# Kernel optimization log

Measured on AMD Instinct MI355X. Metric: run time of the kernel, lower is better.

The kernel has to match this reference:

```python
import jax, jax.numpy as jnp
import numpy as np

BLOCK_K = 32   # BLOCK_K_SIZE_MIN in the original Triton kernel
BLOCK_N = 32   # output-block granularity of the hash


def _hash_indices(random_numbers, num_nb, num_kb, num_red_kb):
    # universal hash of (n_block, k_block) -> reduced k-block index
    r = random_numbers.astype(jnp.uint32)
    nb = jnp.arange(num_nb, dtype=jnp.uint32)[:, None]
    kb = jnp.arange(num_kb, dtype=jnp.uint32)[None, :]
    hv = (kb * r[0] + nb * r[1] + r[2]) ^ r[3]
    return (hv % jnp.uint32(num_red_kb)).astype(jnp.int32)  # [num_nb, num_kb]


def _ssl_forward(x, weight, bias, random_numbers):
    orig_shape = x.shape
    K = orig_shape[-1]
    x2 = x.reshape(-1, K)                       # [M, K]
    N, red_K = weight.shape
    num_kb = K // BLOCK_K
    num_red_kb = red_K // BLOCK_K
    num_nb = N // BLOCK_N
    h = _hash_indices(random_numbers, num_nb, num_kb, num_red_kb)  # [num_nb, num_kb]
    # Gather the virtual full weight from the reduced weight via hash indices.
    wb = weight.reshape(num_nb, BLOCK_N, num_red_kb, BLOCK_K)
    w_full = jnp.take_along_axis(wb, h[:, None, :, None], axis=2)  # [num_nb, BN, num_kb, BK]
    w_full = w_full.reshape(N, K)
    y = x2 @ w_full.T
    if bias is not None:
        y = y + bias
    return y.reshape(*orig_shape[:-1], N)


def setup_inputs() -> dict:
    key = jax.random.key(0)
    k1, k2, k3 = jax.random.split(key, 3)
    in_features, out_features, redn_factor, seed = 8192, 512, 8, 1024
    red_in = ((in_features // redn_factor + BLOCK_K - 1) // BLOCK_K) * BLOCK_K  # 1024
    x = jax.random.normal(k1, (4, 2048, in_features), dtype=jnp.float32)
    bound = 1.0 / np.sqrt(red_in)
    weight = jax.random.uniform(k2, (out_features, red_in), jnp.float32, -bound, bound)
    bias = jax.random.uniform(k3, (out_features,), jnp.float32, -bound, bound)
    rng = np.random.default_rng(seed)
    random_numbers = jnp.asarray(rng.integers(1, 2**31 - 1, size=4), dtype=jnp.int32)
    return {"x": x, "weight": weight, "bias": bias,
            "random_numbers": random_numbers, "redn_factor": redn_factor}


def reference(x, weight, bias, random_numbers, redn_factor):
    return _ssl_forward(x, weight, bias, random_numbers)
```

## Files before the change

kernel.cpp:

```cpp
#include <hip/hip_runtime.h>
#include <hip/hip_bf16.h>
#include <stdint.h>


typedef __bf16 bf16x4_t __attribute__((ext_vector_type(4)));
typedef __bf16 bf16x8_t __attribute__((ext_vector_type(8)));
typedef float f32x4 __attribute__((ext_vector_type(4)));

#define BM 128
#define BN 128
#define BK 32
#define LDSK 40
#define KSPLIT 4

__global__ void init_out(float* __restrict__ Out, const float* __restrict__ Bias,
                         int N, int total4) {
  int i = blockIdx.x * blockDim.x + threadIdx.x;
  if (i < total4) {
    int idx = i << 2;
    int n = idx % N;
    *(f32x4*)(Out + idx) = *(const f32x4*)(Bias + n);
  }
}

__global__ __launch_bounds__(256, 1) void ssl_gemm(
    const float* __restrict__ X,
    const float* __restrict__ W,
    const int* __restrict__ RN,
    float* __restrict__ Out,
    int M, int N, int K, int redK, uint32_t numRedKb, int mTiles, int nTiles) {
  __shared__ __align__(16) __bf16 As[BM * LDSK];
  __shared__ __align__(16) __bf16 Bs[BN * LDSK];

  const uint32_t r0 = (uint32_t)RN[0], r1 = (uint32_t)RN[1];
  const uint32_t r2 = (uint32_t)RN[2], r3 = (uint32_t)RN[3];
  const uint32_t redMask = numRedKb - 1u;
  const bool pow2 = (numRedKb & (numRedKb - 1u)) == 0u;

  const int id = blockIdx.x;
  const int mTile = id % mTiles;
  const int rest = id / mTiles;
  const int nTile = rest % nTiles;
  const int kChunk = rest / nTiles;

  const int tid = threadIdx.x;
  const int wave = tid >> 6;
  const int lane = tid & 63;
  const int wm = wave >> 1, wn = wave & 1;

  const int lRow = tid >> 3;
  const int lCol = (tid & 7) << 2;
  const float* aBase = X + (size_t)(mTile * BM + lRow) * K + lCol;
  const float* bBase = W + (size_t)(nTile * BN + lRow) * redK + lCol;

  auto loadA = [&](int kb, f32x4* r) {
    const float* p = aBase + (size_t)kb * BK;
#pragma unroll
    for (int i = 0; i < 4; ++i)
      r[i] = *(const f32x4*)(p + (size_t)(i * 32) * K);
  };
  auto loadB = [&](int kb, f32x4* r) {
    const uint32_t kk = (uint32_t)kb * r0 + r2;
#pragma unroll
    for (int i = 0; i < 4; ++i) {
      const uint32_t nb = (uint32_t)(nTile * (BN / 32) + i);
      const uint32_t hv = (kk + nb * r1) ^ r3;
      const uint32_t h = pow2 ? (hv & redMask) : (hv % numRedKb);
      r[i] = *(const f32x4*)(bBase + (size_t)(i * 32) * redK + h * 32u);
    }
  };
  auto stage = [&](const f32x4* rA, const f32x4* rB) {
#pragma unroll
    for (int i = 0; i < 4; ++i) {
      bf16x4_t a, b;
#pragma unroll
      for (int j = 0; j < 4; ++j) {
        a[j] = (__bf16)rA[i][j];
        b[j] = (__bf16)rB[i][j];
      }
      *(bf16x4_t*)&As[(i * 32 + lRow) * LDSK + lCol] = a;
      *(bf16x4_t*)&Bs[(i * 32 + lRow) * LDSK + lCol] = b;
    }
  };

  f32x4 acc[4][4] = {};
  auto compute = [&]() {
    bf16x8_t af[4], bfr[4];
    const int kOff = (lane >> 4) << 3;
    const int r16 = lane & 15;
#pragma unroll
    for (int mi = 0; mi < 4; ++mi)
      af[mi] = *(const bf16x8_t*)&As[((wm << 6) + (mi << 4) + r16) * LDSK + kOff];
#pragma unroll
    for (int ni = 0; ni < 4; ++ni)
      bfr[ni] = *(const bf16x8_t*)&Bs[((wn << 6) + (ni << 4) + r16) * LDSK + kOff];
#pragma unroll
    for (int mi = 0; mi < 4; ++mi)
#pragma unroll
      for (int ni = 0; ni < 4; ++ni)
        acc[mi][ni] = __builtin_amdgcn_mfma_f32_16x16x32_bf16(
            af[mi], bfr[ni], acc[mi][ni], 0, 0, 0);
  };

  const int numKb = K / BK;
  const int kbN = numKb / KSPLIT;
  const int kb0 = kChunk * kbN;
  f32x4 a0[4], b0[4], a1[4], b1[4];
  loadA(kb0, a0);
  loadB(kb0, b0);
  for (int i = 0; i < kbN; i += 2) {
    if (i + 1 < kbN) { loadA(kb0 + i + 1, a1); loadB(kb0 + i + 1, b1); }
    __syncthreads();
    stage(a0, b0);
    __syncthreads();
    compute();
    if (i + 2 < kbN) { loadA(kb0 + i + 2, a0); loadB(kb0 + i + 2, b0); }
    __syncthreads();
    stage(a1, b1);
    __syncthreads();
    compute();
  }

  const int mBase = mTile * BM + (wm << 6);
  const int nBase = nTile * BN + (wn << 6);
#pragma unroll
  for (int ni = 0; ni < 4; ++ni) {
    const int n = nBase + (ni << 4) + (lane & 15);
#pragma unroll
    for (int mi = 0; mi < 4; ++mi) {
      const int m0 = mBase + (mi << 4) + ((lane >> 4) << 2);
#pragma unroll
      for (int r = 0; r < 4; ++r)
        unsafeAtomicAdd(&Out[(size_t)(m0 + r) * N + n], acc[mi][ni][r]);
    }
  }
}

extern "C" void kernel_launch(void* const* d_in, const int* in_sizes, int n_in,
                              void* d_out, int out_size, void* d_ws, size_t ws_size,
                              hipStream_t stream) {
  const float* X = (const float*)d_in[0];
  const float* W = (const float*)d_in[1];
  const float* Bias = (const float*)d_in[2];
  const int* RN = (const int*)d_in[3];
  float* Out = (float*)d_out;

  const int N = in_sizes[2];
  const int M = out_size / N;
  const int K = in_sizes[0] / M;
  const int redK = in_sizes[1] / N;
  const uint32_t numRedKb = (uint32_t)(redK / 32);

  const int total4 = out_size / 4;
  init_out<<<(total4 + 255) / 256, 256, 0, stream>>>(Out, Bias, N, total4);

  const int mTiles = M / BM;
  const int nTiles = N / BN;
  dim3 grid(mTiles * nTiles * KSPLIT), block(256);
  ssl_gemm<<<grid, block, 0, stream>>>(X, W, RN, Out,
                                       M, N, K, redK, numRedKb, mTiles, nTiles);
}
```

Measured before the change: 504.1 us.

## Drop LDS staging; have each wave load MFMA fragments directly from global memory

Removes shared-memory staging and all block barriers. Each wave now owns an independent 64x64 output tile and loads its A and B fragments straight from global memory into registers in MFMA layout, converting them to bf16 in registers. The grid becomes per-wave work over M stripes, with N waves and a K split of 2 instead of 4, and launch bounds now allow 2 blocks per CU. The trade-off is that A rows are no longer shared between waves through LDS, so the four waves in a block that share an M stripe each reload X from global memory or cache. The global loads are also narrower and less coalesced, 32-byte pieces per lane across rows.

```diff
diff --git a/kernel.cpp b/kernel.cpp
--- a/kernel.cpp
+++ b/kernel.cpp
@@ -3,97 +3,97 @@
 #include <stdint.h>
 
 
-typedef __bf16 bf16x4_t __attribute__((ext_vector_type(4)));
 typedef __bf16 bf16x8_t __attribute__((ext_vector_type(8)));
 typedef float f32x4 __attribute__((ext_vector_type(4)));
 
-#define BM 128
-#define BN 128
-#define BK 32
-#define LDSK 40
-#define KSPLIT 4
+#define WMT 64
+#define WNT 64
+#define KSPLIT 2
 
 __global__ void init_out(float* __restrict__ Out, const float* __restrict__ Bias,
                          int N, int total4) {
   int i = blockIdx.x * blockDim.x + threadIdx.x;
   if (i < total4) {
     int idx = i << 2;
-    int n = idx % N;
-    *(f32x4*)(Out + idx) = *(const f32x4*)(Bias + n);
+    *(f32x4*)(Out + idx) = *(const f32x4*)(Bias + (idx % N));
   }
 }
 
-__global__ __launch_bounds__(256, 1) void ssl_gemm(
+__global__ __launch_bounds__(256, 2) void ssl_gemm(
     const float* __restrict__ X,
     const float* __restrict__ W,
     const int* __restrict__ RN,
     float* __restrict__ Out,
-    int M, int N, int K, int redK, uint32_t numRedKb, int mTiles, int nTiles) {
-  __shared__ __align__(16) __bf16 As[BM * LDSK];
-  __shared__ __align__(16) __bf16 Bs[BN * LDSK];
-
+    int M, int N, int K, int redK, uint32_t numRedKb, int mStripes, int nW) {
   const uint32_t r0 = (uint32_t)RN[0], r1 = (uint32_t)RN[1];
   const uint32_t r2 = (uint32_t)RN[2], r3 = (uint32_t)RN[3];
   const uint32_t redMask = numRedKb - 1u;
   const bool pow2 = (numRedKb & (numRedKb - 1u)) == 0u;
 
   const int id = blockIdx.x;
-  const int mTile = id % mTiles;
-  const int rest = id / mTiles;
-  const int nTile = rest % nTiles;
-  const int kChunk = rest / nTiles;
+  const int s = id % mStripes;
+  const int j = id / mStripes;
+  const int wave = threadIdx.x >> 6;
+  const int lane = threadIdx.x & 63;
+  const int v = (j << 2) + wave;
+  const int nIdx = v % nW;
+  const int kChunk = v / nW;
 
-  const int tid = threadIdx.x;
-  const int wave = tid >> 6;
-  const int lane = tid & 63;
-  const int wm = wave >> 1, wn = wave & 1;
+  const int m0 = s * WMT;
+  const int n0 = nIdx * WNT;
+  const int r16 = lane & 15;
+  const int kq = lane >> 4;
 
-  const int lRow = tid >> 3;
-  const int lCol = (tid & 7) << 2;
-  const float* aBase = X + (size_t)(mTile * BM + lRow) * K + lCol;
-  const float* bBase = W + (size_t)(nTile * BN + lRow) * redK + lCol;
+  const float* aP[4];
+  const float* bP[4];
+#pragma unroll
+  for (int mi = 0; mi < 4; ++mi)
+    aP[mi] = X + (size_t)(m0 + (mi << 4) + r16) * K + (kq << 3);
+#pragma unroll
+  for (int ni = 0; ni < 4; ++ni)
+    bP[ni] = W + (size_t)(n0 + (ni << 4) + r16) * redK + (kq << 3);
 
-  auto loadA = [&](int kb, f32x4* r) {
-    const float* p = aBase + (size_t)kb * BK;
+  const uint32_t nb0 = (uint32_t)(n0 >> 5);
+  const uint32_t nb1 = nb0 + 1u;
+
+  f32x4 acc[4][4] = {};
+
+  auto loadStep = [&](int kb, f32x4 (&A)[4][2], f32x4 (&B)[4][2]) {
+    const uint32_t kk = (uint32_t)kb * r0 + r2;
+    uint32_t h0 = (kk + nb0 * r1) ^ r3;
+    uint32_t h1 = (kk + nb1 * r1) ^ r3;
+    h0 = pow2 ? (h0 & redMask) : (h0 % numRedKb);
+    h1 = pow2 ? (h1 & redMask) : (h1 % numRedKb);
+    const size_t ka = (size_t)kb << 5;
 #pragma unroll
-    for (int i = 0; i < 4; ++i)
-      r[i] = *(const f32x4*)(p + (size_t)(i * 32) * K);
-  };
-  auto loadB = [&](int kb, f32x4* r) {
-    const uint32_t kk = (uint32_t)kb * r0 + r2;
+    for (int mi = 0; mi < 4; ++mi) {
+      A[mi][0] = *(const f32x4*)(aP[mi] + ka);
+      A[mi][1] = *(const f32x4*)(aP[mi] + ka + 4);
+    }
 #pragma unroll
-    for (int i = 0; i < 4; ++i) {
-      const uint32_t nb = (uint32_t)(nTile * (BN / 32) + i);
-      const uint32_t hv = (kk + nb * r1) ^ r3;
-      const uint32_t h = pow2 ? (hv & redMask) : (hv % numRedKb);
-      r[i] = *(const f32x4*)(bBase + (size_t)(i * 32) * redK + h * 32u);
-    }
-  };
-  auto stage = [&](const f32x4* rA, const f32x4* rB) {
-#pragma unroll
-    for (int i = 0; i < 4; ++i) {
-      bf16x4_t a, b;
-#pragma unroll
-      for (int j = 0; j < 4; ++j) {
-        a[j] = (__bf16)rA[i][j];
-        b[j] = (__bf16)rB[i][j];
-      }
-      *(bf16x4_t*)&As[(i * 32 + lRow) * LDSK + lCol] = a;
-      *(bf16x4_t*)&Bs[(i * 32 + lRow) * LDSK + lCol] = b;
+    for (int ni = 0; ni < 4; ++ni) {
+      const size_t kc = (size_t)((ni < 2 ? h0 : h1) << 5);
+      B[ni][0] = *(const f32x4*)(bP[ni] + kc);
+      B[ni][1] = *(const f32x4*)(bP[ni] + kc + 4);
     }
   };
 
-  f32x4 acc[4][4] = {};
-  auto compute = [&]() {
+  auto computeStep = [&](const f32x4 (&A)[4][2], const f32x4 (&B)[4][2]) {
     bf16x8_t af[4], bfr[4];
-    const int kOff = (lane >> 4) << 3;
-    const int r16 = lane & 15;
 #pragma unroll
     for (int mi = 0; mi < 4; ++mi)
-      af[mi] = *(const bf16x8_t*)&As[((wm << 6) + (mi << 4) + r16) * LDSK + kOff];
+#pragma unroll
+      for (int q = 0; q < 4; ++q) {
+        af[mi][q] = (__bf16)A[mi][0][q];
+        af[mi][q + 4] = (__bf16)A[mi][1][q];
+      }
 #pragma unroll
     for (int ni = 0; ni < 4; ++ni)
-      bfr[ni] = *(const bf16x8_t*)&Bs[((wn << 6) + (ni << 4) + r16) * LDSK + kOff];
+#pragma unroll
+      for (int q = 0; q < 4; ++q) {
+        bfr[ni][q] = (__bf16)B[ni][0][q];
+        bfr[ni][q + 4] = (__bf16)B[ni][1][q];
+      }
 #pragma unroll
     for (int mi = 0; mi < 4; ++mi)
 #pragma unroll
@@ -102,36 +102,28 @@
             af[mi], bfr[ni], acc[mi][ni], 0, 0, 0);
   };
 
-  const int numKb = K / BK;
-  const int kbN = numKb / KSPLIT;
+  const int kbTotal = K / 32;
+  const int kbN = kbTotal / KSPLIT;
   const int kb0 = kChunk * kbN;
-  f32x4 a0[4], b0[4], a1[4], b1[4];
-  loadA(kb0, a0);
-  loadB(kb0, b0);
+
+  f32x4 Pa[4][2], Pb[4][2], Qa[4][2], Qb[4][2];
+  loadStep(kb0, Pa, Pb);
   for (int i = 0; i < kbN; i += 2) {
-    if (i + 1 < kbN) { loadA(kb0 + i + 1, a1); loadB(kb0 + i + 1, b1); }
-    __syncthreads();
-    stage(a0, b0);
-    __syncthreads();
-    compute();
-    if (i + 2 < kbN) { loadA(kb0 + i + 2, a0); loadB(kb0 + i + 2, b0); }
-    __syncthreads();
-    stage(a1, b1);
-    __syncthreads();
-    compute();
+    loadStep(kb0 + i + 1, Qa, Qb);
+    computeStep(Pa, Pb);
+    if (i + 2 < kbN) loadStep(kb0 + i + 2, Pa, Pb);
+    computeStep(Qa, Qb);
   }
 
-  const int mBase = mTile * BM + (wm << 6);
-  const int nBase = nTile * BN + (wn << 6);
 #pragma unroll
   for (int ni = 0; ni < 4; ++ni) {
-    const int n = nBase + (ni << 4) + (lane & 15);
+    const int n = n0 + (ni << 4) + r16;
 #pragma unroll
     for (int mi = 0; mi < 4; ++mi) {
-      const int m0 = mBase + (mi << 4) + ((lane >> 4) << 2);
+      const int mBase = m0 + (mi << 4) + (kq << 2);
 #pragma unroll
       for (int r = 0; r < 4; ++r)
-        unsafeAtomicAdd(&Out[(size_t)(m0 + r) * N + n], acc[mi][ni][r]);
+        unsafeAtomicAdd(&Out[(size_t)(mBase + r) * N + n], acc[mi][ni][r]);
     }
   }
 }
@@ -154,9 +146,9 @@
   const int total4 = out_size / 4;
   init_out<<<(total4 + 255) / 256, 256, 0, stream>>>(Out, Bias, N, total4);
 
-  const int mTiles = M / BM;
-  const int nTiles = N / BN;
-  dim3 grid(mTiles * nTiles * KSPLIT), block(256);
-  ssl_gemm<<<grid, block, 0, stream>>>(X, W, RN, Out,
-                                       M, N, K, redK, numRedKb, mTiles, nTiles);
+  const int mStripes = M / WMT;
+  const int nW = N / WNT;
+  const int blocks = mStripes * ((nW * KSPLIT) / 4);
+  ssl_gemm<<<blocks, 256, 0, stream>>>(X, W, RN, Out,
+                                       M, N, K, redK, numRedKb, mStripes, nW);
 }
```

Measured after the change: 740.2 us. 1.47x slower.
